# Optimization experiments

Measured on AMD Instinct MI355X. Metric: run time of the kernel, lower is better.

The kernel has to match this reference:

```python
import jax, jax.numpy as jnp
import numpy as np

D = 768           # input_dim == slot_dim
H, DH = 8, 64     # encoder attention heads / head dim (x-transformers defaults)
INNER = 4 * D     # ff_mult=4 GLU inner dim
EPS = 1e-8
N_ITERS = 3
SCALE = D ** -0.5


def _ln(x, g, b):
    m = jnp.mean(x, axis=-1, keepdims=True)
    v = jnp.var(x, axis=-1, keepdims=True)
    return (x - m) / jnp.sqrt(v + 1e-5) * g + b


def setup_inputs() -> dict:
    key = jax.random.key(0)
    ks = jax.random.split(key, 16)
    w = lambda i, shape, s=0.02: jax.random.normal(ks[i], shape, jnp.float32) * s
    return dict(
        x=jax.random.normal(ks[0], (32, 1024, D), jnp.float32),
        noise=jax.random.normal(ks[1], (32, 16, D), jnp.float32),
        init_mu=jax.random.normal(ks[2], (D,), jnp.float32),
        init_log_sigma=w(3, (D,), 0.05),
        Wk=w(4, (D, D)), Wv=w(5, (D, D)), Wq=w(6, (D, D)),
        ni_g=jnp.ones(D), ni_b=jnp.zeros(D),       # norm_input
        ns_g=jnp.ones(D), ns_b=jnp.zeros(D),       # norm_slots
        nica_g=jnp.ones(D), nica_b=jnp.zeros(D),   # norm_ica
        ln1_g=jnp.ones(D), ln1_b=jnp.zeros(D),     # encoder attn pre-norm
        Wq_a=w(7, (D, H * DH)), Wk_a=w(8, (D, H * DH)),
        Wv_a=w(9, (D, H * DH)), Wo_a=w(10, (H * DH, D)),
        ln2_g=jnp.ones(D), ln2_b=jnp.zeros(D),     # encoder ff pre-norm
        W1=w(11, (D, 2 * INNER)), W2=w(12, (INNER, D)),
        lnf_g=jnp.ones(D), lnf_b=jnp.zeros(D),     # encoder final norm
    )


def _inv_cross_attn(q, k, v):
    # softmax over the SLOT axis (dim i), then renormalize over keys j
    dots = jnp.einsum('bid,bjd->bij', q, k) * SCALE
    attn = jax.nn.softmax(dots, axis=1) + EPS
    attn = attn / jnp.sum(attn, axis=-1, keepdims=True)
    updates = jnp.einsum('bjd,bij->bid', v, attn)
    return updates, attn


def _encoder(h, ln1_g, ln1_b, Wq_a, Wk_a, Wv_a, Wo_a, ln2_g, ln2_b, W1, W2, lnf_g, lnf_b):
    b, n, _ = h.shape
    a = _ln(h, ln1_g, ln1_b)
    q = (a @ Wq_a).reshape(b, n, H, DH)
    k = (a @ Wk_a).reshape(b, n, H, DH)
    v = (a @ Wv_a).reshape(b, n, H, DH)
    scores = jnp.einsum('bihd,bjhd->bhij', q, k) * (DH ** -0.5)
    p = jax.nn.softmax(scores, axis=-1)
    o = jnp.einsum('bhij,bjhd->bihd', p, v).reshape(b, n, H * DH)
    h = h + o @ Wo_a
    f = _ln(h, ln2_g, ln2_b)
    u, g = jnp.split(f @ W1, 2, axis=-1)
    h = h + (u * jax.nn.silu(g)) @ W2
    return _ln(h, lnf_g, lnf_b)


def reference(x, noise, init_mu, init_log_sigma, Wk, Wv, Wq,
              ni_g, ni_b, ns_g, ns_b, nica_g, nica_b,
              ln1_g, ln1_b, Wq_a, Wk_a, Wv_a, Wo_a,
              ln2_g, ln2_b, W1, W2, lnf_g, lnf_b):
    xn = _ln(x, ni_g, ni_b)
    k = xn @ Wk
    v = xn @ Wv
    slots = init_mu + jnp.exp(init_log_sigma) * noise  # [b, n_slots, d]

    def step(slots):
        q = _ln(slots, ns_g, ns_b) @ Wq
        updates, attn = _inv_cross_attn(q, k, v)
        slots = _ln(slots + updates, nica_g, nica_b)
        slots = _encoder(slots, ln1_g, ln1_b, Wq_a, Wk_a, Wv_a, Wo_a,
                         ln2_g, ln2_b, W1, W2, lnf_g, lnf_b)
        return slots, attn

    for _ in range(N_ITERS):
        slots, _ = step(slots)
    slots, attn = step(slots)
    attn_map = jnp.transpose(attn, (0, 2, 1))  # b n hw -> b hw n
    return slots, attn_map
```

## Files before the change

### kernel.cpp

```cpp
#include <hip/hip_runtime.h>
#include <hip/hip_bf16.h>
#include <stdint.h>

typedef _Float16 f16;
typedef __attribute__((ext_vector_type(8))) _Float16 f16x8;
typedef __attribute__((ext_vector_type(4))) _Float16 f16x4;
typedef __attribute__((ext_vector_type(4))) float f32x4;

#define GLOBAL_AS __attribute__((address_space(1)))
#define LDS_AS __attribute__((address_space(3)))

#define D_DIM 768
#define NTOK 1024
#define NSLOT 16
#define NB 32
#define NTOT (NB*NTOK)
#define HDIM 512
#define INNER 3072
#define SCALE_D 0.03608439182435161f
#define SCALE_H 0.125f

template<int OUT>
__global__ __launch_bounds__(256) void mgemm64_k(
    const f16* __restrict__ A, const f16* __restrict__ Bt,
    void* __restrict__ Cout, int M, int N, int K, int Kc)
{
  __shared__ __align__(16) f16 As[64*128];
  __shared__ __align__(16) f16 Bs[64*128];
  const int tid = threadIdx.x;
  const int lane = tid & 63;
  const int wave = tid >> 6;
  const int m0 = blockIdx.x*64, n0 = blockIdx.y*64;
  const int kbeg = blockIdx.z * Kc;
  const int wm = (wave>>1)*32, wn = (wave&1)*32;
  const int quad = lane>>4, l16 = lane&15;

  const int sr = tid>>2;
  const int sc = (tid&3)*8;
  const f16* gA = A  + (size_t)(m0+sr)*K + kbeg + sc;
  const f16* gB = Bt + (size_t)(n0+sr)*K + kbeg + sc;
  LDS_AS f16* lA = (LDS_AS f16*)&As[(size_t)tid*8];
  LDS_AS f16* lB = (LDS_AS f16*)&Bs[(size_t)tid*8];

  const f16* fA0 = &As[(wm + l16)*32 + quad*8];
  const f16* fB0 = &Bs[(wn + l16)*32 + quad*8];

  f32x4 acc[2][2] = {};

  for (int k0 = 0; k0 < Kc; k0 += 128){
    #pragma unroll
    for (int p=0;p<4;++p){
      __builtin_amdgcn_global_load_lds((const GLOBAL_AS void*)(gA + k0 + p*32),
                                       (LDS_AS void*)(lA + (size_t)p*2048), 16, 0, 0);
      __builtin_amdgcn_global_load_lds((const GLOBAL_AS void*)(gB + k0 + p*32),
                                       (LDS_AS void*)(lB + (size_t)p*2048), 16, 0, 0);
    }
    __syncthreads();
    #pragma unroll
    for (int p=0;p<4;++p){
      f16x8 a0 = *(const f16x8*)(fA0 + p*2048);
      f16x8 a1 = *(const f16x8*)(fA0 + p*2048 + 16*32);
      f16x8 b0 = *(const f16x8*)(fB0 + p*2048);
      f16x8 b1 = *(const f16x8*)(fB0 + p*2048 + 16*32);
      acc[0][0] = __builtin_amdgcn_mfma_f32_16x16x32_f16(a0,b0,acc[0][0],0,0,0);
      acc[0][1] = __builtin_amdgcn_mfma_f32_16x16x32_f16(a0,b1,acc[0][1],0,0,0);
      acc[1][0] = __builtin_amdgcn_mfma_f32_16x16x32_f16(a1,b0,acc[1][0],0,0,0);
      acc[1][1] = __builtin_amdgcn_mfma_f32_16x16x32_f16(a1,b1,acc[1][1],0,0,0);
    }
    __syncthreads();
  }
  #pragma unroll
  for (int mt=0;mt<2;++mt){
    #pragma unroll
    for (int nt=0;nt<2;++nt){
      int gm = m0 + wm + mt*16 + quad*4;
      int gn = n0 + wn + nt*16 + l16;
      #pragma unroll
      for (int r=0;r<4;++r){
        float c = acc[mt][nt][r];
        size_t idx = (size_t)(gm+r)*N + gn;
        if (OUT==1) ((f16*)Cout)[idx] = (f16)c;
        else        atomicAdd(&((float*)Cout)[idx], c);
      }
    }
  }
}

__global__ __launch_bounds__(256) void w1glu_k(
    const f16* __restrict__ A, const f16* __restrict__ W1T,
    f16* __restrict__ act, int M)
{
  __shared__ __align__(16) f16 As[64*128];
  __shared__ __align__(16) f16 Bu[64*128];
  __shared__ __align__(16) f16 Bg[64*128];
  const int K = 768;
  const int tid = threadIdx.x;
  const int lane = tid & 63;
  const int wave = tid >> 6;
  const int m0 = blockIdx.x*64, n0 = blockIdx.y*64;
  const int wm = (wave>>1)*32, wn = (wave&1)*32;
  const int quad = lane>>4, l16 = lane&15;

  const int sr = tid>>2;
  const int sc = (tid&3)*8;
  const f16* gA  = A   + (size_t)(m0+sr)*K + sc;
  const f16* gBu = W1T + (size_t)(n0+sr)*K + sc;
  const f16* gBg = W1T + (size_t)(3072+n0+sr)*K + sc;
  LDS_AS f16* lA  = (LDS_AS f16*)&As[(size_t)tid*8];
  LDS_AS f16* lBu = (LDS_AS f16*)&Bu[(size_t)tid*8];
  LDS_AS f16* lBg = (LDS_AS f16*)&Bg[(size_t)tid*8];

  const f16* fA0 = &As[(wm + l16)*32 + quad*8];
  const f16* fU0 = &Bu[(wn + l16)*32 + quad*8];
  const f16* fG0 = &Bg[(wn + l16)*32 + quad*8];

  f32x4 accU[2][2] = {};
  f32x4 accG[2][2] = {};

  for (int k0 = 0; k0 < K; k0 += 128){
    #pragma unroll
    for (int p=0;p<4;++p){
      __builtin_amdgcn_global_load_lds((const GLOBAL_AS void*)(gA  + k0 + p*32),
                                       (LDS_AS void*)(lA  + (size_t)p*2048), 16, 0, 0);
      __builtin_amdgcn_global_load_lds((const GLOBAL_AS void*)(gBu + k0 + p*32),
                                       (LDS_AS void*)(lBu + (size_t)p*2048), 16, 0, 0);
      __builtin_amdgcn_global_load_lds((const GLOBAL_AS void*)(gBg + k0 + p*32),
                                       (LDS_AS void*)(lBg + (size_t)p*2048), 16, 0, 0);
    }
    __syncthreads();
    #pragma unroll
    for (int p=0;p<4;++p){
      f16x8 a0 = *(const f16x8*)(fA0 + p*2048);
      f16x8 a1 = *(const f16x8*)(fA0 + p*2048 + 16*32);
      f16x8 u0 = *(const f16x8*)(fU0 + p*2048);
      f16x8 u1 = *(const f16x8*)(fU0 + p*2048 + 16*32);
      f16x8 g0 = *(const f16x8*)(fG0 + p*2048);
      f16x8 g1 = *(const f16x8*)(fG0 + p*2048 + 16*32);
      accU[0][0] = __builtin_amdgcn_mfma_f32_16x16x32_f16(a0,u0,accU[0][0],0,0,0);
      accU[0][1] = __builtin_amdgcn_mfma_f32_16x16x32_f16(a0,u1,accU[0][1],0,0,0);
      accU[1][0] = __builtin_amdgcn_mfma_f32_16x16x32_f16(a1,u0,accU[1][0],0,0,0);
      accU[1][1] = __builtin_amdgcn_mfma_f32_16x16x32_f16(a1,u1,accU[1][1],0,0,0);
      accG[0][0] = __builtin_amdgcn_mfma_f32_16x16x32_f16(a0,g0,accG[0][0],0,0,0);
      accG[0][1] = __builtin_amdgcn_mfma_f32_16x16x32_f16(a0,g1,accG[0][1],0,0,0);
      accG[1][0] = __builtin_amdgcn_mfma_f32_16x16x32_f16(a1,g0,accG[1][0],0,0,0);
      accG[1][1] = __builtin_amdgcn_mfma_f32_16x16x32_f16(a1,g1,accG[1][1],0,0,0);
    }
    __syncthreads();
  }
  #pragma unroll
  for (int mt=0;mt<2;++mt){
    #pragma unroll
    for (int nt=0;nt<2;++nt){
      int gm = m0 + wm + mt*16 + quad*4;
      int gn = n0 + wn + nt*16 + l16;
      #pragma unroll
      for (int r=0;r<4;++r){
        float u = accU[mt][nt][r];
        float g = accG[mt][nt][r];
        float sg = g / (1.0f + __expf(-g));
        act[(size_t)(gm+r)*INNER + gn] = (f16)(u*sg);
      }
    }
  }
}

__global__ __launch_bounds__(256) void dots_k(
    const f16* __restrict__ Q,
    const f16* __restrict__ Xn,
    f16* __restrict__ attn,
    float* __restrict__ rsPart)
{
  __shared__ __align__(16) f16 qf[16*768];
  __shared__ __align__(16) f16 ks[64*128];
  __shared__ float rpart[4][16];
  const int b = blockIdx.x, jt = blockIdx.y;
  const int tid = threadIdx.x;
  const int lane = tid & 63;
  const int w = tid >> 6;
  const int quad = lane>>4, l16 = lane&15;

  #pragma unroll
  for (int c=0;c<6;++c){
    int p = c*256 + tid;
    int ki = p >> 6, qd = (p >> 4) & 3, rw = p & 15;
    f16x8 v = *(const f16x8*)(Q + ((size_t)(b*NSLOT+rw))*D_DIM + ki*32 + qd*8);
    *(f16x8*)&qf[(size_t)p*8] = v;
  }

  const f16* gK = Xn + ((size_t)(b*NTOK + jt*64 + (tid>>2)))*D_DIM + (tid&3)*8;
  LDS_AS f16* lK = (LDS_AS f16*)&ks[(size_t)tid*8];

  f32x4 acc = {};
  for (int it=0; it<6; ++it){
    #pragma unroll
    for (int p=0;p<4;++p)
      __builtin_amdgcn_global_load_lds((const GLOBAL_AS void*)(gK + it*128 + p*32),
                                       (LDS_AS void*)(lK + (size_t)p*2048), 16, 0, 0);
    __syncthreads();
    #pragma unroll
    for (int p=0;p<4;++p){
      f16x8 a  = *(const f16x8*)&qf[(((size_t)(it*4+p)*4 + quad)*16 + l16)*8];
      f16x8 bf = *(const f16x8*)&ks[(size_t)p*2048 + (w*16+l16)*32 + quad*8];
      acc = __builtin_amdgcn_mfma_f32_16x16x32_f16(a, bf, acc, 0, 0, 0);
    }
    __syncthreads();
  }

  float v0 = acc[0]*SCALE_D, v1 = acc[1]*SCALE_D, v2 = acc[2]*SCALE_D, v3 = acc[3]*SCALE_D;
  float mx = fmaxf(fmaxf(v0,v1), fmaxf(v2,v3));
  mx = fmaxf(mx, __shfl_xor(mx, 16));
  mx = fmaxf(mx, __shfl_xor(mx, 32));
  float e0 = __expf(v0-mx), e1 = __expf(v1-mx), e2 = __expf(v2-mx), e3 = __expf(v3-mx);
  float s = e0+e1+e2+e3;
  s += __shfl_xor(s, 16);
  s += __shfl_xor(s, 32);
  float inv = 1.0f/s;
  float a0 = e0*inv + 1e-8f, a1 = e1*inv + 1e-8f, a2 = e2*inv + 1e-8f, a3 = e3*inv + 1e-8f;

  int jcol = jt*64 + w*16 + l16;
  int ibase = b*NSLOT + quad*4;
  attn[(size_t)(ibase+0)*NTOK + jcol] = (f16)a0;
  attn[(size_t)(ibase+1)*NTOK + jcol] = (f16)a1;
  attn[(size_t)(ibase+2)*NTOK + jcol] = (f16)a2;
  attn[(size_t)(ibase+3)*NTOK + jcol] = (f16)a3;

  float t0=a0, t1=a1, t2=a2, t3=a3;
  #pragma unroll
  for (int m=1;m<16;m<<=1){
    t0 += __shfl_xor(t0, m);
    t1 += __shfl_xor(t1, m);
    t2 += __shfl_xor(t2, m);
    t3 += __shfl_xor(t3, m);
  }
  if (l16 == 0){
    rpart[w][quad*4+0] = t0;
    rpart[w][quad*4+1] = t1;
    rpart[w][quad*4+2] = t2;
    rpart[w][quad*4+3] = t3;
  }
  __syncthreads();
  if (tid < 16){
    float ss = rpart[0][tid] + rpart[1][tid] + rpart[2][tid] + rpart[3][tid];
    rsPart[(size_t)((b*16 + jt)<<4) + tid] = ss;
  }
}

__global__ __launch_bounds__(256) void attnv_k(
    const f16* __restrict__ attn,
    const float* __restrict__ rsPart,
    const f16* __restrict__ XnT,
    const f16* __restrict__ WvT,
    float* __restrict__ accb)
{
  __shared__ __align__(16) f16 Asl[16*128];
  __shared__ __align__(16) f16 Bsl[64*128];
  __shared__ float rsum[16];
  __shared__ __align__(16) f16 tl[16][80];
  const int b = blockIdx.x, d0 = blockIdx.y*64;
  const int tid = threadIdx.x;
  const int lane = tid & 63;
  const int w = tid >> 6;
  const int quad = lane>>4, l16 = lane&15;

  if (tid < 16){
    float s = 0.f;
    #pragma unroll
    for (int jt=0;jt<16;++jt) s += rsPart[(size_t)((b*16 + jt)<<4) + tid];
    rsum[tid] = s;
  }

  const int pa = tid>>6, ta = tid&63;
  const f16* gA = attn + ((size_t)(b*NSLOT + (ta>>2)))*NTOK + pa*32 + (ta&3)*8;
  LDS_AS f16* lA = (LDS_AS f16*)&Asl[(size_t)pa*512 + ta*8];
  const f16* gB = XnT + ((size_t)(d0 + (tid>>2)))*NTOT + b*NTOK + (tid&3)*8;
  LDS_AS f16* lB = (LDS_AS f16*)&Bsl[(size_t)tid*8];

  f32x4 acc = {};
  for (int it=0; it<8; ++it){
    __builtin_amdgcn_global_load_lds((const GLOBAL_AS void*)(gA + it*128),
                                     (LDS_AS void*)lA, 16, 0, 0);
    #pragma unroll
    for (int p=0;p<4;++p)
      __builtin_amdgcn_global_load_lds((const GLOBAL_AS void*)(gB + it*128 + p*32),
                                       (LDS_AS void*)(lB + (size_t)p*2048), 16, 0, 0);
    __syncthreads();
    #pragma unroll
    for (int p=0;p<4;++p){
      f16x8 a  = *(const f16x8*)&Asl[(size_t)p*512 + l16*32 + quad*8];
      f16x8 bf = *(const f16x8*)&Bsl[(size_t)p*2048 + (w*16+l16)*32 + quad*8];
      acc = __builtin_amdgcn_mfma_f32_16x16x32_f16(a, bf, acc, 0, 0, 0);
    }
    __syncthreads();
  }
  const int dloc = w*16 + l16;
  #pragma unroll
  for (int r=0;r<4;++r)
    tl[quad*4+r][dloc] = (f16)(acc[r] / rsum[quad*4+r]);
  __syncthreads();
  f16x8 af0 = *(const f16x8*)&tl[l16][quad*8];
  f16x8 af1 = *(const f16x8*)&tl[l16][32 + quad*8];
  const f16* bp = WvT + (size_t)l16*D_DIM + d0 + quad*8;
  float* up = accb + (size_t)(b*NSLOT + quad*4)*D_DIM + l16;
  #pragma unroll
  for (int j=0;j<12;++j){
    int n0 = (w*12 + j)*16;
    f16x8 b0 = *(const f16x8*)(bp + (size_t)n0*D_DIM);
    f16x8 b1 = *(const f16x8*)(bp + (size_t)n0*D_DIM + 32);
    f32x4 c = {};
    c = __builtin_amdgcn_mfma_f32_16x16x32_f16(af0, b0, c, 0,0,0);
    c = __builtin_amdgcn_mfma_f32_16x16x32_f16(af1, b1, c, 0,0,0);
    #pragma unroll
    for (int r=0;r<4;++r) atomicAdd(up + (size_t)r*D_DIM + n0, c[r]);
  }
}

__global__ __launch_bounds__(256) void lnw_k(
    const float* __restrict__ X,
    const float* __restrict__ g, const float* __restrict__ bb,
    f16* __restrict__ out)
{
  const int lane = threadIdx.x & 63;
  const size_t row = (size_t)blockIdx.x*4 + (threadIdx.x>>6);
  const float* x = X + row*D_DIM;
  float4 v[3]; float s=0.f, ss=0.f;
  #pragma unroll
  for (int t=0;t<3;++t){
    v[t] = *(const float4*)(x + lane*4 + t*256);
    s  += v[t].x+v[t].y+v[t].z+v[t].w;
    ss += v[t].x*v[t].x+v[t].y*v[t].y+v[t].z*v[t].z+v[t].w*v[t].w;
  }
  #pragma unroll
  for (int m=1;m<64;m<<=1){ s += __shfl_xor(s,m); ss += __shfl_xor(ss,m); }
  float mean = s*(1.0f/768.0f);
  float inv  = rsqrtf(ss*(1.0f/768.0f) - mean*mean + 1e-5f);
  #pragma unroll
  for (int t=0;t<3;++t){
    int c0 = lane*4 + t*256;
    float4 gg = *(const float4*)(g + c0);
    float4 bv = *(const float4*)(bb + c0);
    f16x4 h4;
    h4.x = (f16)((v[t].x-mean)*inv*gg.x + bv.x);
    h4.y = (f16)((v[t].y-mean)*inv*gg.y + bv.y);
    h4.z = (f16)((v[t].z-mean)*inv*gg.z + bv.z);
    h4.w = (f16)((v[t].w-mean)*inv*gg.w + bv.w);
    *(f16x4*)(out + row*D_DIM + c0) = h4;
  }
}

template<bool WACC>
__global__ __launch_bounds__(256) void lnlnw_k(
    const float* __restrict__ X,
    const float* __restrict__ g1, const float* __restrict__ b1,
    const float* __restrict__ g2, const float* __restrict__ b2,
    float* __restrict__ out1, f16* __restrict__ out2, float* __restrict__ acc)
{
  const int lane = threadIdx.x & 63;
  const size_t row = (size_t)blockIdx.x*4 + (threadIdx.x>>6);
  const float* x = X + row*D_DIM;
  float4 v[3]; float s=0.f, ss=0.f;
  #pragma unroll
  for (int t=0;t<3;++t){
    v[t] = *(const float4*)(x + lane*4 + t*256);
    s  += v[t].x+v[t].y+v[t].z+v[t].w;
    ss += v[t].x*v[t].x+v[t].y*v[t].y+v[t].z*v[t].z+v[t].w*v[t].w;
  }
  #pragma unroll
  for (int m=1;m<64;m<<=1){ s += __shfl_xor(s,m); ss += __shfl_xor(ss,m); }
  float mean = s*(1.0f/768.0f);
  float inv  = rsqrtf(ss*(1.0f/768.0f) - mean*mean + 1e-5f);
  float y[3][4]; float s2=0.f, ss2=0.f;
  #pragma unroll
  for (int t=0;t<3;++t){
    int c0 = lane*4 + t*256;
    float4 gg = *(const float4*)(g1 + c0);
    float4 bv = *(const float4*)(b1 + c0);
    y[t][0] = (v[t].x-mean)*inv*gg.x + bv.x;
    y[t][1] = (v[t].y-mean)*inv*gg.y + bv.y;
    y[t][2] = (v[t].z-mean)*inv*gg.z + bv.z;
    y[t][3] = (v[t].w-mean)*inv*gg.w + bv.w;
    float4 o = { y[t][0], y[t][1], y[t][2], y[t][3] };
    *(float4*)(out1 + row*D_DIM + c0) = o;
    if (WACC) *(float4*)(acc + row*D_DIM + c0) = o;
    s2  += y[t][0]+y[t][1]+y[t][2]+y[t][3];
    ss2 += y[t][0]*y[t][0]+y[t][1]*y[t][1]+y[t][2]*y[t][2]+y[t][3]*y[t][3];
  }
  #pragma unroll
  for (int m=1;m<64;m<<=1){ s2 += __shfl_xor(s2,m); ss2 += __shfl_xor(ss2,m); }
  float mean2 = s2*(1.0f/768.0f);
  float inv2  = rsqrtf(ss2*(1.0f/768.0f) - mean2*mean2 + 1e-5f);
  #pragma unroll
  for (int t=0;t<3;++t){
    int c0 = lane*4 + t*256;
    float4 gg = *(const float4*)(g2 + c0);
    float4 bv = *(const float4*)(b2 + c0);
    f16x4 h4;
    h4.x = (f16)((y[t][0]-mean2)*inv2*gg.x + bv.x);
    h4.y = (f16)((y[t][1]-mean2)*inv2*gg.y + bv.y);
    h4.z = (f16)((y[t][2]-mean2)*inv2*gg.z + bv.z);
    h4.w = (f16)((y[t][3]-mean2)*inv2*gg.w + bv.w);
    *(f16x4*)(out2 + row*D_DIM + c0) = h4;
  }
}

__global__ __launch_bounds__(256) void slotsinit_k(
    const float* __restrict__ noise, const float* __restrict__ mu,
    const float* __restrict__ ls,
    const float* __restrict__ nsg, const float* __restrict__ nsb,
    float* __restrict__ slots, float* __restrict__ accb, f16* __restrict__ tmp2)
{
  const int lane = threadIdx.x & 63;
  const size_t row = (size_t)blockIdx.x*4 + (threadIdx.x>>6);
  float4 v[3]; float s=0.f, ss=0.f;
  #pragma unroll
  for (int t=0;t<3;++t){
    int c0 = lane*4 + t*256;
    float4 nz = *(const float4*)(noise + row*D_DIM + c0);
    float4 m4 = *(const float4*)(mu + c0);
    float4 l4 = *(const float4*)(ls + c0);
    v[t].x = m4.x + __expf(l4.x)*nz.x;
    v[t].y = m4.y + __expf(l4.y)*nz.y;
    v[t].z = m4.z + __expf(l4.z)*nz.z;
    v[t].w = m4.w + __expf(l4.w)*nz.w;
    *(float4*)(slots + row*D_DIM + c0) = v[t];
    *(float4*)(accb  + row*D_DIM + c0) = v[t];
    s  += v[t].x+v[t].y+v[t].z+v[t].w;
    ss += v[t].x*v[t].x+v[t].y*v[t].y+v[t].z*v[t].z+v[t].w*v[t].w;
  }
  #pragma unroll
  for (int m=1;m<64;m<<=1){ s += __shfl_xor(s,m); ss += __shfl_xor(ss,m); }
  float mean = s*(1.0f/768.0f);
  float inv  = rsqrtf(ss*(1.0f/768.0f) - mean*mean + 1e-5f);
  #pragma unroll
  for (int t=0;t<3;++t){
    int c0 = lane*4 + t*256;
    float4 gg = *(const float4*)(nsg + c0);
    float4 bv = *(const float4*)(nsb + c0);
    f16x4 h4;
    h4.x = (f16)((v[t].x-mean)*inv*gg.x + bv.x);
    h4.y = (f16)((v[t].y-mean)*inv*gg.y + bv.y);
    h4.z = (f16)((v[t].z-mean)*inv*gg.z + bv.z);
    h4.w = (f16)((v[t].w-mean)*inv*gg.w + bv.w);
    *(f16x4*)(tmp2 + row*D_DIM + c0) = h4;
  }
}

__global__ __launch_bounds__(256) void encwo_k(
    const f16* __restrict__ QA, const f16* __restrict__ KA,
    const f16* __restrict__ VA, int QSTR,
    const f16* __restrict__ WoT,
    float* __restrict__ hb)
{
  __shared__ float qs[16][68], ks[16][68], vs[16][68], ps[16][20];
  __shared__ __align__(16) f16 ol[16][80];
  const int b = blockIdx.x, h = blockIdx.y;
  const int tid = threadIdx.x;
  {
    int i = tid>>4, dd=(tid&15)*4;
    size_t base = ((size_t)(b*NSLOT+i))*QSTR + h*64 + dd;
    f16x4 uq = *(const f16x4*)(QA + base);
    f16x4 uk = *(const f16x4*)(KA + base);
    f16x4 uv = *(const f16x4*)(VA + base);
    float4 fq = { (float)uq.x, (float)uq.y, (float)uq.z, (float)uq.w };
    float4 fk = { (float)uk.x, (float)uk.y, (float)uk.z, (float)uk.w };
    float4 fv = { (float)uv.x, (float)uv.y, (float)uv.z, (float)uv.w };
    *(float4*)&qs[i][dd]=fq; *(float4*)&ks[i][dd]=fk; *(float4*)&vs[i][dd]=fv;
  }
  __syncthreads();
  {
    int i = tid>>4, j = tid&15;
    float s=0.f;
    #pragma unroll 8
    for (int d=0; d<64; ++d) s += qs[i][d]*ks[j][d];
    ps[i][j] = s*SCALE_H;
  }
  __syncthreads();
  if (tid < 16){
    int i = tid;
    float mx=-1e30f;
    #pragma unroll
    for (int j=0;j<16;++j) mx = fmaxf(mx, ps[i][j]);
    float sm=0.f;
    #pragma unroll
    for (int j=0;j<16;++j){ float e=__expf(ps[i][j]-mx); ps[i][j]=e; sm+=e; }
    float inv=1.0f/sm;
    #pragma unroll
    for (int j=0;j<16;++j) ps[i][j]*=inv;
  }
  __syncthreads();
  {
    int i = tid>>4, dq=(tid&15)*4;
    float a0=0,a1=0,a2=0,a3=0;
    #pragma unroll
    for (int j=0;j<16;++j){
      float p = ps[i][j];
      a0+=p*vs[j][dq+0]; a1+=p*vs[j][dq+1]; a2+=p*vs[j][dq+2]; a3+=p*vs[j][dq+3];
    }
    f16x4 o4 = { (f16)a0, (f16)a1, (f16)a2, (f16)a3 };
    *(f16x4*)&ol[i][dq] = o4;
  }
  __syncthreads();
  const int lane = tid & 63, w = tid>>6, quad = lane>>4, l16 = lane&15;
  f16x8 af0 = *(const f16x8*)&ol[l16][quad*8];
  f16x8 af1 = *(const f16x8*)&ol[l16][32 + quad*8];
  const f16* bp = WoT + (size_t)l16*HDIM + h*64 + quad*8;
  float* hp = hb + (size_t)(b*NSLOT + quad*4)*D_DIM + l16;
  #pragma unroll
  for (int j=0;j<12;++j){
    int n0 = (w*12 + j)*16;
    f16x8 b0 = *(const f16x8*)(bp + (size_t)n0*HDIM);
    f16x8 b1 = *(const f16x8*)(bp + (size_t)n0*HDIM + 32);
    f32x4 c = {};
    c = __builtin_amdgcn_mfma_f32_16x16x32_f16(af0, b0, c, 0,0,0);
    c = __builtin_amdgcn_mfma_f32_16x16x32_f16(af1, b1, c, 0,0,0);
    #pragma unroll
    for (int r=0;r<4;++r) atomicAdd(hp + (size_t)r*D_DIM + n0, c[r]);
  }
}

__global__ __launch_bounds__(256) void transp_k(
    const f16* __restrict__ in, f16* __restrict__ out, int R, int C)
{
  __shared__ f16 T[64][72];
  const int m0 = blockIdx.x*64, d0 = blockIdx.y*64;
  const int tid = threadIdx.x;
  {
    int r = tid>>2, c = (tid&3)*16;
    const f16* p = in + (size_t)(m0+r)*C + d0 + c;
    *(f16x8*)&T[r][c]   = *(const f16x8*)p;
    *(f16x8*)&T[r][c+8] = *(const f16x8*)(p+8);
  }
  __syncthreads();
  {
    int dd = tid>>2, mq = (tid&3)*16;
    f16 v[16];
    #pragma unroll
    for (int e=0;e<16;++e) v[e] = T[mq+e][dd];
    f16* p = out + (size_t)(d0+dd)*R + m0 + mq;
    *(f16x8*)p     = *(f16x8*)&v[0];
    *(f16x8*)(p+8) = *(f16x8*)&v[8];
  }
}

__global__ __launch_bounds__(256) void prep_k(
    const float* __restrict__ Wv,   const float* __restrict__ Wq_a,
    const float* __restrict__ Wk_a, const float* __restrict__ Wv_a,
    const float* __restrict__ Wo_a, const float* __restrict__ W1,
    const float* __restrict__ W2,   const float* __restrict__ Wk,
    const float* __restrict__ Wq,
    f16* __restrict__ WvT, f16* __restrict__ WqkvT, f16* __restrict__ WoaT,
    f16* __restrict__ W1T, f16* __restrict__ W2T,
    f16* __restrict__ Wkf, f16* __restrict__ Wqf)
{
  __shared__ float t[32][33];
  int bid = blockIdx.x;
  const float* src; f16* dst; int R, C; bool tr = true;
  if      (bid < 576)  {              src=Wv;   dst=WvT;             R=768;  C=768; }
  else if (bid < 960)  { bid-=576;    src=Wq_a; dst=WqkvT;           R=768;  C=512; }
  else if (bid < 1344) { bid-=960;    src=Wk_a; dst=WqkvT+512*768;   R=768;  C=512; }
  else if (bid < 1728) { bid-=1344;   src=Wv_a; dst=WqkvT+1024*768;  R=768;  C=512; }
  else if (bid < 2112) { bid-=1728;   src=Wo_a; dst=WoaT;            R=512;  C=768; }
  else if (bid < 6720) { bid-=2112;   src=W1;   dst=W1T;             R=768;  C=6144; }
  else if (bid < 9024) { bid-=6720;   src=W2;   dst=W2T;             R=3072; C=768; }
  else if (bid < 9600) { bid-=9024;   src=Wk;   dst=Wkf;             R=768;  C=768; tr=false; }
  else                 { bid-=9600;   src=Wq;   dst=Wqf;             R=768;  C=768; tr=false; }
  const int tpr = C/32;
  const int r0 = (bid / tpr)*32, c0 = (bid % tpr)*32;
  const int lc = threadIdx.x & 31, g8 = threadIdx.x >> 5;
  if (tr){
    #pragma unroll
    for (int s=0;s<4;++s){
      int r = g8*4 + s;
      t[r][lc] = src[(size_t)(r0+r)*C + c0+lc];
    }
    __syncthreads();
    #pragma unroll
    for (int s=0;s<4;++s){
      int c = g8*4 + s;
      dst[(size_t)(c0+c)*R + r0+lc] = (f16)t[lc][c];
    }
  } else {
    #pragma unroll
    for (int s=0;s<4;++s){
      int r = g8*4 + s;
      dst[(size_t)(r0+r)*C + c0+lc] = (f16)src[(size_t)(r0+r)*C + c0+lc];
    }
  }
}

__global__ __launch_bounds__(256) void attnout_k(
    const f16* __restrict__ attn, const float* __restrict__ rsPart,
    float* __restrict__ out)
{
  __shared__ float rsum[16];
  const int bid = blockIdx.x, tid = threadIdx.x;
  const int b = bid >> 6;
  if (tid < 16){
    float s = 0.f;
    #pragma unroll
    for (int jt=0;jt<16;++jt) s += rsPart[(size_t)((b*16+jt)<<4) + tid];
    rsum[tid] = s;
  }
  __syncthreads();
  int idx = bid*256 + tid;
  int i = idx & 15;
  int j = (idx >> 4) & 1023;
  out[idx] = (float)attn[((size_t)(b*NSLOT)+i)*NTOK + j] / rsum[i];
}

extern "C" void kernel_launch(void* const* d_in, const int* in_sizes, int n_in,
                              void* d_out, int out_size, void* d_ws, size_t ws_size,
                              hipStream_t stream) {
  const float* x        = (const float*)d_in[0];
  const float* noise    = (const float*)d_in[1];
  const float* init_mu  = (const float*)d_in[2];
  const float* init_ls  = (const float*)d_in[3];
  const float* Wk       = (const float*)d_in[4];
  const float* Wv       = (const float*)d_in[5];
  const float* Wq       = (const float*)d_in[6];
  const float* ni_g     = (const float*)d_in[7];
  const float* ni_b     = (const float*)d_in[8];
  const float* ns_g     = (const float*)d_in[9];
  const float* ns_b     = (const float*)d_in[10];
  const float* nica_g   = (const float*)d_in[11];
  const float* nica_b   = (const float*)d_in[12];
  const float* ln1_g    = (const float*)d_in[13];
  const float* ln1_b    = (const float*)d_in[14];
  const float* Wq_a     = (const float*)d_in[15];
  const float* Wk_a     = (const float*)d_in[16];
  const float* Wv_a     = (const float*)d_in[17];
  const float* Wo_a     = (const float*)d_in[18];
  const float* ln2_g    = (const float*)d_in[19];
  const float* ln2_b    = (const float*)d_in[20];
  const float* W1       = (const float*)d_in[21];
  const float* W2       = (const float*)d_in[22];
  const float* lnf_g    = (const float*)d_in[23];
  const float* lnf_b    = (const float*)d_in[24];

  char* w = (char*)d_ws;
  size_t off = 0;
  auto alloc = [&](size_t bytes)->char*{
    char* p = w + off; off += (bytes + 255) & ~(size_t)255; return p;
  };
  f16* xn_h  = (f16*)alloc((size_t)NTOT*D_DIM*2);
  f16* xnT_h = (f16*)alloc((size_t)D_DIM*NTOT*2);
  f16* Wkf   = (f16*)alloc((size_t)768*768*2);
  f16* Wqf   = (f16*)alloc((size_t)768*768*2);
  f16* BtQK  = (f16*)alloc((size_t)768*768*2);
  f16* WvT   = (f16*)alloc((size_t)768*768*2);
  f16* WqkvT = (f16*)alloc((size_t)1536*768*2);
  f16* WoaT  = (f16*)alloc((size_t)768*512*2);
  f16* W1T   = (f16*)alloc((size_t)6144*768*2);
  f16* W2T   = (f16*)alloc((size_t)768*3072*2);
  float* slots = (float*)alloc(512*768*4);
  float* hbuf  = (float*)alloc(512*768*4);
  float* accb  = (float*)alloc(512*768*4);
  f16* tmp_h  = (f16*)alloc(512*768*2);
  f16* tmp2_h = (f16*)alloc(512*768*2);
  f16* q_h    = (f16*)alloc(512*768*2);
  f16* qkv_h  = (f16*)alloc((size_t)512*1536*2);
  f16* act_h  = (f16*)alloc((size_t)512*3072*2);
  f16* attn_h = (f16*)alloc((size_t)NB*NSLOT*NTOK*2);
  float* rsPart = (float*)alloc((size_t)32*16*16*4);

  prep_k<<<10176, 256, 0, stream>>>(Wv, Wq_a, Wk_a, Wv_a, Wo_a, W1, W2, Wk, Wq,
                                    WvT, WqkvT, WoaT, W1T, W2T, Wkf, Wqf);

  mgemm64_k<1><<<dim3(12, 12, 1), 256, 0, stream>>>(Wkf, Wqf, BtQK, 768, 768, 768, 768);

  lnw_k<<<NTOT/4, 256, 0, stream>>>(x, ni_g, ni_b, xn_h);
  transp_k<<<dim3(NTOT/64, D_DIM/64), 256, 0, stream>>>(xn_h, xnT_h, NTOT, D_DIM);

  slotsinit_k<<<128, 256, 0, stream>>>(noise, init_mu, init_ls, ns_g, ns_b,
                                       slots, accb, tmp2_h);

  for (int it=0; it<4; ++it){
    mgemm64_k<1><<<dim3(8, 12, 1), 256, 0, stream>>>(tmp2_h, BtQK, q_h, 512, 768, 768, 768);
    dots_k<<<dim3(NB, 16), 256, 0, stream>>>(q_h, xn_h, attn_h, rsPart);
    attnv_k<<<dim3(NB, 12), 256, 0, stream>>>(attn_h, rsPart, xnT_h, WvT, accb);
    lnlnw_k<false><<<128, 256, 0, stream>>>(accb, nica_g, nica_b, ln1_g, ln1_b,
                                            hbuf, tmp_h, nullptr);
    mgemm64_k<1><<<dim3(8, 24, 1), 256, 0, stream>>>(tmp_h, WqkvT, qkv_h, 512, 1536, 768, 768);
    encwo_k<<<dim3(NB, 8), 256, 0, stream>>>(qkv_h, qkv_h + 512, qkv_h + 1024, 1536,
                                             WoaT, hbuf);
    lnw_k<<<128, 256, 0, stream>>>(hbuf, ln2_g, ln2_b, tmp_h);
    w1glu_k<<<dim3(8, 48), 256, 0, stream>>>(tmp_h, W1T, act_h, 512);
    mgemm64_k<2><<<dim3(8, 12, 4), 256, 0, stream>>>(act_h, W2T, hbuf, 512, 768, 3072, 768);
    lnlnw_k<true><<<128, 256, 0, stream>>>(hbuf, lnf_g, lnf_b, ns_g, ns_b,
                                           slots, tmp2_h, accb);
  }

  hipMemcpyAsync(d_out, slots, (size_t)512*768*4, hipMemcpyDeviceToDevice, stream);
  attnout_k<<<NB*NTOK*NSLOT/256, 256, 0, stream>>>(attn_h, rsPart, (float*)d_out + 512*768);
}
```

Before: 713.3 us.

## Unfuse Wv and Wo projections from attention kernels into separate GEMMs

The attention-times-V kernel and the encoder attention kernel used to apply the Wv and Wo projections inline, with per-block MFMA tiles and many fp32 atomicAdds. They now write fp16 intermediates, and dedicated tiled GEMM launches (a plain-store variant and a split-K atomic variant) do the projections. The residual add for slots moves into the layernorm kernel, which removes the accb initialization copies. The last iteration writes straight to the output, dropping the final memcpy. This adds kernel launches and intermediate buffer traffic in exchange for far fewer scattered atomics and better GEMM efficiency.

```diff
diff --git a/kernel.cpp b/kernel.cpp
--- a/kernel.cpp
+++ b/kernel.cpp
@@ -79,8 +79,9 @@
       for (int r=0;r<4;++r){
         float c = acc[mt][nt][r];
         size_t idx = (size_t)(gm+r)*N + gn;
-        if (OUT==1) ((f16*)Cout)[idx] = (f16)c;
-        else        atomicAdd(&((float*)Cout)[idx], c);
+        if (OUT==0)      ((float*)Cout)[idx] = c;
+        else if (OUT==1) ((f16*)Cout)[idx] = (f16)c;
+        else             atomicAdd(&((float*)Cout)[idx], c);
       }
     }
   }
@@ -249,13 +250,11 @@
     const f16* __restrict__ attn,
     const float* __restrict__ rsPart,
     const f16* __restrict__ XnT,
-    const f16* __restrict__ WvT,
-    float* __restrict__ accb)
+    f16* __restrict__ t_out)
 {
   __shared__ __align__(16) f16 Asl[16*128];
   __shared__ __align__(16) f16 Bsl[64*128];
   __shared__ float rsum[16];
-  __shared__ __align__(16) f16 tl[16][80];
   const int b = blockIdx.x, d0 = blockIdx.y*64;
   const int tid = threadIdx.x;
   const int lane = tid & 63;
@@ -292,25 +291,11 @@
     }
     __syncthreads();
   }
-  const int dloc = w*16 + l16;
-  #pragma unroll
-  for (int r=0;r<4;++r)
-    tl[quad*4+r][dloc] = (f16)(acc[r] / rsum[quad*4+r]);
-  __syncthreads();
-  f16x8 af0 = *(const f16x8*)&tl[l16][quad*8];
-  f16x8 af1 = *(const f16x8*)&tl[l16][32 + quad*8];
-  const f16* bp = WvT + (size_t)l16*D_DIM + d0 + quad*8;
-  float* up = accb + (size_t)(b*NSLOT + quad*4)*D_DIM + l16;
-  #pragma unroll
-  for (int j=0;j<12;++j){
-    int n0 = (w*12 + j)*16;
-    f16x8 b0 = *(const f16x8*)(bp + (size_t)n0*D_DIM);
-    f16x8 b1 = *(const f16x8*)(bp + (size_t)n0*D_DIM + 32);
-    f32x4 c = {};
-    c = __builtin_amdgcn_mfma_f32_16x16x32_f16(af0, b0, c, 0,0,0);
-    c = __builtin_amdgcn_mfma_f32_16x16x32_f16(af1, b1, c, 0,0,0);
-    #pragma unroll
-    for (int r=0;r<4;++r) atomicAdd(up + (size_t)r*D_DIM + n0, c[r]);
+  int dcol = d0 + w*16 + l16;
+  #pragma unroll
+  for (int r=0;r<4;++r){
+    int i = quad*4 + r;
+    t_out[(size_t)(b*NSLOT + i)*D_DIM + dcol] = (f16)(acc[r] / rsum[i]);
   }
 }
 
@@ -347,20 +332,27 @@
   }
 }
 
-template<bool WACC>
+template<bool ADD>
 __global__ __launch_bounds__(256) void lnlnw_k(
-    const float* __restrict__ X,
+    const float* __restrict__ X, const float* __restrict__ X2,
     const float* __restrict__ g1, const float* __restrict__ b1,
     const float* __restrict__ g2, const float* __restrict__ b2,
-    float* __restrict__ out1, f16* __restrict__ out2, float* __restrict__ acc)
+    float* __restrict__ out1, f16* __restrict__ out2)
 {
   const int lane = threadIdx.x & 63;
   const size_t row = (size_t)blockIdx.x*4 + (threadIdx.x>>6);
   const float* x = X + row*D_DIM;
+  const float* x2 = X2 + row*D_DIM;
   float4 v[3]; float s=0.f, ss=0.f;
   #pragma unroll
   for (int t=0;t<3;++t){
-    v[t] = *(const float4*)(x + lane*4 + t*256);
+    int c0 = lane*4 + t*256;
+    float4 a = *(const float4*)(x + c0);
+    if (ADD){
+      float4 b = *(const float4*)(x2 + c0);
+      a.x+=b.x; a.y+=b.y; a.z+=b.z; a.w+=b.w;
+    }
+    v[t]=a;
     s  += v[t].x+v[t].y+v[t].z+v[t].w;
     ss += v[t].x*v[t].x+v[t].y*v[t].y+v[t].z*v[t].z+v[t].w*v[t].w;
   }
@@ -380,7 +372,6 @@
     y[t][3] = (v[t].w-mean)*inv*gg.w + bv.w;
     float4 o = { y[t][0], y[t][1], y[t][2], y[t][3] };
     *(float4*)(out1 + row*D_DIM + c0) = o;
-    if (WACC) *(float4*)(acc + row*D_DIM + c0) = o;
     s2  += y[t][0]+y[t][1]+y[t][2]+y[t][3];
     ss2 += y[t][0]*y[t][0]+y[t][1]*y[t][1]+y[t][2]*y[t][2]+y[t][3]*y[t][3];
   }
@@ -406,7 +397,7 @@
     const float* __restrict__ noise, const float* __restrict__ mu,
     const float* __restrict__ ls,
     const float* __restrict__ nsg, const float* __restrict__ nsb,
-    float* __restrict__ slots, float* __restrict__ accb, f16* __restrict__ tmp2)
+    float* __restrict__ slots, f16* __restrict__ tmp2)
 {
   const int lane = threadIdx.x & 63;
   const size_t row = (size_t)blockIdx.x*4 + (threadIdx.x>>6);
@@ -422,7 +413,6 @@
     v[t].z = m4.z + __expf(l4.z)*nz.z;
     v[t].w = m4.w + __expf(l4.w)*nz.w;
     *(float4*)(slots + row*D_DIM + c0) = v[t];
-    *(float4*)(accb  + row*D_DIM + c0) = v[t];
     s  += v[t].x+v[t].y+v[t].z+v[t].w;
     ss += v[t].x*v[t].x+v[t].y*v[t].y+v[t].z*v[t].z+v[t].w*v[t].w;
   }
@@ -444,14 +434,12 @@
   }
 }
 
-__global__ __launch_bounds__(256) void encwo_k(
+__global__ __launch_bounds__(256) void encattn_k(
     const f16* __restrict__ QA, const f16* __restrict__ KA,
     const f16* __restrict__ VA, int QSTR,
-    const f16* __restrict__ WoT,
-    float* __restrict__ hb)
+    f16* __restrict__ O)
 {
   __shared__ float qs[16][68], ks[16][68], vs[16][68], ps[16][20];
-  __shared__ __align__(16) f16 ol[16][80];
   const int b = blockIdx.x, h = blockIdx.y;
   const int tid = threadIdx.x;
   {
@@ -495,25 +483,8 @@
       float p = ps[i][j];
       a0+=p*vs[j][dq+0]; a1+=p*vs[j][dq+1]; a2+=p*vs[j][dq+2]; a3+=p*vs[j][dq+3];
     }
-    f16x4 o4 = { (f16)a0, (f16)a1, (f16)a2, (f16)a3 };
-    *(f16x4*)&ol[i][dq] = o4;
-  }
-  __syncthreads();
-  const int lane = tid & 63, w = tid>>6, quad = lane>>4, l16 = lane&15;
-  f16x8 af0 = *(const f16x8*)&ol[l16][quad*8];
-  f16x8 af1 = *(const f16x8*)&ol[l16][32 + quad*8];
-  const f16* bp = WoT + (size_t)l16*HDIM + h*64 + quad*8;
-  float* hp = hb + (size_t)(b*NSLOT + quad*4)*D_DIM + l16;
-  #pragma unroll
-  for (int j=0;j<12;++j){
-    int n0 = (w*12 + j)*16;
-    f16x8 b0 = *(const f16x8*)(bp + (size_t)n0*HDIM);
-    f16x8 b1 = *(const f16x8*)(bp + (size_t)n0*HDIM + 32);
-    f32x4 c = {};
-    c = __builtin_amdgcn_mfma_f32_16x16x32_f16(af0, b0, c, 0,0,0);
-    c = __builtin_amdgcn_mfma_f32_16x16x32_f16(af1, b1, c, 0,0,0);
-    #pragma unroll
-    for (int r=0;r<4;++r) atomicAdd(hp + (size_t)r*D_DIM + n0, c[r]);
+    size_t base = ((size_t)(b*NSLOT+i))*HDIM + h*64 + dq;
+    O[base+0]=(f16)a0; O[base+1]=(f16)a1; O[base+2]=(f16)a2; O[base+3]=(f16)a3;
   }
 }
 
@@ -653,11 +624,13 @@
   f16* W2T   = (f16*)alloc((size_t)768*3072*2);
   float* slots = (float*)alloc(512*768*4);
   float* hbuf  = (float*)alloc(512*768*4);
-  float* accb  = (float*)alloc(512*768*4);
+  float* upd   = (float*)alloc(512*768*4);
   f16* tmp_h  = (f16*)alloc(512*768*2);
   f16* tmp2_h = (f16*)alloc(512*768*2);
   f16* q_h    = (f16*)alloc(512*768*2);
+  f16* t_h    = (f16*)alloc(512*768*2);
   f16* qkv_h  = (f16*)alloc((size_t)512*1536*2);
+  f16* o_h    = (f16*)alloc(512*512*2);
   f16* act_h  = (f16*)alloc((size_t)512*3072*2);
   f16* attn_h = (f16*)alloc((size_t)NB*NSLOT*NTOK*2);
   float* rsPart = (float*)alloc((size_t)32*16*16*4);
@@ -671,24 +644,25 @@
   transp_k<<<dim3(NTOT/64, D_DIM/64), 256, 0, stream>>>(xn_h, xnT_h, NTOT, D_DIM);
 
   slotsinit_k<<<128, 256, 0, stream>>>(noise, init_mu, init_ls, ns_g, ns_b,
-                                       slots, accb, tmp2_h);
+                                       slots, tmp2_h);
 
   for (int it=0; it<4; ++it){
     mgemm64_k<1><<<dim3(8, 12, 1), 256, 0, stream>>>(tmp2_h, BtQK, q_h, 512, 768, 768, 768);
     dots_k<<<dim3(NB, 16), 256, 0, stream>>>(q_h, xn_h, attn_h, rsPart);
-    attnv_k<<<dim3(NB, 12), 256, 0, stream>>>(attn_h, rsPart, xnT_h, WvT, accb);
-    lnlnw_k<false><<<128, 256, 0, stream>>>(accb, nica_g, nica_b, ln1_g, ln1_b,
-                                            hbuf, tmp_h, nullptr);
+    attnv_k<<<dim3(NB, 12), 256, 0, stream>>>(attn_h, rsPart, xnT_h, t_h);
+    mgemm64_k<0><<<dim3(8, 12, 1), 256, 0, stream>>>(t_h, WvT, upd, 512, 768, 768, 768);
+    lnlnw_k<true><<<128, 256, 0, stream>>>(slots, upd, nica_g, nica_b, ln1_g, ln1_b,
+                                           hbuf, tmp_h);
     mgemm64_k<1><<<dim3(8, 24, 1), 256, 0, stream>>>(tmp_h, WqkvT, qkv_h, 512, 1536, 768, 768);
-    encwo_k<<<dim3(NB, 8), 256, 0, stream>>>(qkv_h, qkv_h + 512, qkv_h + 1024, 1536,
-                                             WoaT, hbuf);
+    encattn_k<<<dim3(NB, 8), 256, 0, stream>>>(qkv_h, qkv_h + 512, qkv_h + 1024, 1536, o_h);
+    mgemm64_k<2><<<dim3(8, 12, 2), 256, 0, stream>>>(o_h, WoaT, hbuf, 512, 768, 512, 256);
     lnw_k<<<128, 256, 0, stream>>>(hbuf, ln2_g, ln2_b, tmp_h);
     w1glu_k<<<dim3(8, 48), 256, 0, stream>>>(tmp_h, W1T, act_h, 512);
     mgemm64_k<2><<<dim3(8, 12, 4), 256, 0, stream>>>(act_h, W2T, hbuf, 512, 768, 3072, 768);
-    lnlnw_k<true><<<128, 256, 0, stream>>>(hbuf, lnf_g, lnf_b, ns_g, ns_b,
-                                           slots, tmp2_h, accb);
-  }
-
-  hipMemcpyAsync(d_out, slots, (size_t)512*768*4, hipMemcpyDeviceToDevice, stream);
+    float* out1 = (it==3) ? (float*)d_out : slots;
+    lnlnw_k<false><<<128, 256, 0, stream>>>(hbuf, nullptr, lnf_g, lnf_b, ns_g, ns_b,
+                                            out1, tmp2_h);
+  }
+
   attnout_k<<<NB*NTOK*NSLOT/256, 256, 0, stream>>>(attn_h, rsPart, (float*)d_out + 512*768);
 }
```

Result: faster. 627.9 us (-12.0%).
